# Performance work log

Measured on AMD Instinct MI355X. Metric: run time of the kernel, lower is better.

Reference implementation:

```python
import jax, jax.numpy as jnp
import numpy as np

B, S, D, H = 2, 2048, 1024, 16
HD = D // H  # 64


def setup_inputs() -> dict:
    key = jax.random.key(0)
    ks = jax.random.split(key, 10)
    inp = {
        "queries": jax.random.normal(ks[0], (B, S, D), dtype=jnp.float32),
        "keys": jax.random.normal(ks[1], (B, S, D), dtype=jnp.float32),
        "values": jax.random.normal(ks[2], (B, S, D), dtype=jnp.float32),
        "attention_mask": jax.random.randint(ks[3], (B, S), 0, 2, dtype=jnp.int32),
        # Linear params (torch nn.Linear: y = x @ W.T + b), scaled like default init
        "Wq": jax.random.normal(ks[4], (D, D), dtype=jnp.float32) / np.sqrt(D),
        "bq": jnp.zeros((D,), dtype=jnp.float32),
        "Wk": jax.random.normal(ks[5], (D, D), dtype=jnp.float32) / np.sqrt(D),
        "bk": jnp.zeros((D,), dtype=jnp.float32),
        "Wv": jax.random.normal(ks[6], (D, D), dtype=jnp.float32) / np.sqrt(D),
        "bv": jnp.zeros((D,), dtype=jnp.float32),
    }
    return inp


def _split_heads(x):
    # torch.chunk along last dim + stack(dim=1) == reshape + transpose
    b, s, d = x.shape
    return x.reshape(b, s, H, HD).transpose(0, 2, 1, 3)  # [B,H,S,hd]


def reference(queries, keys, values, attention_mask, Wq, bq, Wk, bk, Wv, bv):
    q = jax.nn.relu(queries @ Wq.T + bq)
    k = jax.nn.relu(keys @ Wk.T + bk)
    v = jax.nn.relu(values @ Wv.T + bv)
    qh, kh, vh = _split_heads(q), _split_heads(k), _split_heads(v)
    score = jnp.einsum("bhqd,bhkd->bhqk", qh, kh) / jnp.sqrt(jnp.float32(HD))
    # enc mask: [B,1,S,1] broadcast over key dim — masks whole query rows where mask==0
    row_mask = (attention_mask == 0)[:, None, :, None]
    score = jnp.where(row_mask, jnp.float32(-1e9), score)
    attn = jax.nn.softmax(score, axis=-1)
    a = jnp.einsum("bhqk,bhkd->bhqd", attn, vh)  # [B,H,S,hd]
    # faithful to original: permute(0,1,3,2) then reshape to (B,S,D)
    a = a.transpose(0, 1, 3, 2).reshape(q.shape[0], q.shape[1], q.shape[2])
    return a + queries
```

## Files before the change

### kernel.cpp

```cpp
#include <hip/hip_runtime.h>
#include <hip/hip_bf16.h>

#define DEV __device__ __forceinline__

typedef __attribute__((ext_vector_type(8))) short short8;
typedef __attribute__((ext_vector_type(4))) float f32x4;

#define MFMA16(a, b, c) __builtin_amdgcn_mfma_f32_16x16x32_bf16((a), (b), (c), 0, 0, 0)

static constexpr int B_ = 2, S_ = 2048, D_ = 1024, H_ = 16, HD_ = 64;
static constexpr long NX = (long)B_ * S_ * D_;
static constexpr long NW = (long)D_ * D_;

DEV short f2bf(float f) {
    __hip_bfloat16 h = __float2bfloat16(f);
    union { __hip_bfloat16 hh; short s; } u;
    u.hh = h;
    return u.s;
}

DEV float bf2f(short s) {
    union { float f; unsigned u; } x;
    x.u = ((unsigned)(unsigned short)s) << 16;
    return x.f;
}

DEV unsigned cvtpk(float a, float b) {
    unsigned r;
    asm("v_cvt_pk_bf16_f32 %0, %1, %2" : "=v"(r) : "v"(a), "v"(b));
    return r;
}

DEV short8 pk8(float4 lo, float4 hi) {
    union { short8 s8; unsigned u[4]; } u;
    u.u[0] = cvtpk(lo.x, lo.y);
    u.u[1] = cvtpk(lo.z, lo.w);
    u.u[2] = cvtpk(hi.x, hi.y);
    u.u[3] = cvtpk(hi.z, hi.w);
    return u.s8;
}

DEV short8 ld8(const short* p) { return *(const short8*)p; }

DEV void gld16(const short* g, short* l) {
    __builtin_amdgcn_global_load_lds(
        (const __attribute__((address_space(1))) unsigned int*)g,
        (__attribute__((address_space(3))) unsigned int*)l, 16, 0, 0);
}

__global__ __launch_bounds__(256) void convert_w(
    const float* __restrict__ wq, const float* __restrict__ wk, const float* __restrict__ wv,
    short* __restrict__ wqb, short* __restrict__ wkb, short* __restrict__ wvb) {
    long tid = (long)blockIdx.x * 256 + threadIdx.x;
    long e = tid * 4;
    const float* src; short* dst; long off;
    if      (e < NW)     { src = wq; dst = wqb; off = e; }
    else if (e < 2*NW)   { src = wk; dst = wkb; off = e - NW; }
    else                 { src = wv; dst = wvb; off = e - 2*NW; }
    float4 f = *(const float4*)(src + off);
    short4 o;
    o.x = f2bf(f.x); o.y = f2bf(f.y); o.z = f2bf(f.z); o.w = f2bf(f.w);
    *(short4*)(dst + off) = o;
}

__global__ __launch_bounds__(256) void gemm_bias_relu(
    const float* __restrict__ X0, const float* __restrict__ X1, const float* __restrict__ X2,
    const short* __restrict__ W0, const short* __restrict__ W1, const short* __restrict__ W2,
    const float* __restrict__ b0, const float* __restrict__ b1, const float* __restrict__ b2,
    short* __restrict__ O0, short* __restrict__ O1, short* __restrict__ O2) {
    __shared__ short As[2][128 * 32];
    __shared__ short Bs[2][128 * 32];

    const int bid = blockIdx.x;
    const int tl  = (bid & 7) * 96 + (bid >> 3);
    const int bx  = tl & 7;
    const int by  = (tl >> 3) & 31;
    const int z   = tl >> 8;

    const float* X   = (z == 0) ? X0 : (z == 1) ? X1 : X2;
    const short* W   = (z == 0) ? W0 : (z == 1) ? W1 : W2;
    const float* bia = (z == 0) ? b0 : (z == 1) ? b1 : b2;
    short*       Out = (z == 0) ? O0 : (z == 1) ? O1 : O2;

    const int tid  = threadIdx.x;
    const int wid  = tid >> 6;
    const int lane = tid & 63;
    const int id   = lane & 15;
    const int quad = lane >> 4;
    const int m0 = by * 128;
    const int n0 = bx * 128;
    const int wm = (wid >> 1) * 64;
    const int wn = (wid & 1) * 64;

    const float* Ag = X + (long)(m0 + wid * 32 + (lane >> 2)) * D_ + (lane & 3) * 8;
    const short* Bg0 = W + (long)(n0 + wid * 32 + (lane >> 2)) * D_ + (lane & 3) * 8;
    const int offW = wid * 1024;
    const int aDst = offW + lane * 8;

    f32x4 acc[4][4] = {};

    {
        float4 l0 = *(const float4*)(Ag);
        float4 h0 = *(const float4*)(Ag + 4);
        float4 l1 = *(const float4*)(Ag + 16 * D_);
        float4 h1 = *(const float4*)(Ag + 16 * D_ + 4);
        gld16(Bg0,            &Bs[0][offW]);
        gld16(Bg0 + 16 * D_,  &Bs[0][offW + 512]);
        *(short8*)(&As[0][aDst])       = pk8(l0, h0);
        *(short8*)(&As[0][aDst + 512]) = pk8(l1, h1);
    }

    for (int kk = 0; kk < D_; kk += 32) {
        const int cur = (kk >> 5) & 1;
        const int nxt = cur ^ 1;
        const bool pre = (kk + 32 < D_);
        float4 l0, h0, l1, h1;
        __syncthreads();
        if (pre) {
            l0 = *(const float4*)(Ag + kk + 32);
            h0 = *(const float4*)(Ag + kk + 36);
            l1 = *(const float4*)(Ag + 16 * D_ + kk + 32);
            h1 = *(const float4*)(Ag + 16 * D_ + kk + 36);
            gld16(Bg0 + kk + 32,            &Bs[nxt][offW]);
            gld16(Bg0 + 16 * D_ + kk + 32,  &Bs[nxt][offW + 512]);
        }

        short8 af[4], bf[4];
#pragma unroll
        for (int i = 0; i < 4; i++) af[i] = ld8(&As[cur][(wm + 16*i + id) * 32 + quad * 8]);
#pragma unroll
        for (int j = 0; j < 4; j++) bf[j] = ld8(&Bs[cur][(wn + 16*j + id) * 32 + quad * 8]);
#pragma unroll
        for (int i = 0; i < 4; i++)
#pragma unroll
            for (int j = 0; j < 4; j++)
                acc[i][j] = MFMA16(af[i], bf[j], acc[i][j]);

        if (pre) {
            *(short8*)(&As[nxt][aDst])       = pk8(l0, h0);
            *(short8*)(&As[nxt][aDst + 512]) = pk8(l1, h1);
        }
    }

#pragma unroll
    for (int j = 0; j < 4; j++) {
        int col = n0 + wn + 16*j + id;
        float bj = bia[col];
#pragma unroll
        for (int i = 0; i < 4; i++) {
#pragma unroll
            for (int r = 0; r < 4; r++) {
                int row = m0 + wm + 16*i + quad*4 + r;
                float val = fmaxf(acc[i][j][r] + bj, 0.f);
                Out[(long)row * D_ + col] = f2bf(val);
            }
        }
    }
}

__global__ __launch_bounds__(256) void transpose_v(const short* __restrict__ Vp,
                                                   short* __restrict__ VT) {
    __shared__ short tile[64 * 64];
    const int bh = blockIdx.y;
    const int b = bh >> 4, h = bh & 15;
    const int s0 = blockIdx.x * 64;
    const int t = threadIdx.x;
#pragma unroll
    for (int it = 0; it < 2; it++) {
        int row = (t >> 3) + 32 * it;
        int u   = t & 7;
        short8 d = ld8(Vp + (long)(b * S_ + s0 + row) * D_ + h * HD_ + u * 8);
        *(short8*)(&tile[row * 64 + (u ^ ((row >> 3) & 7)) * 8]) = d;
    }
    __syncthreads();
#pragma unroll
    for (int it = 0; it < 2; it++) {
        int e  = (t >> 3) + 32 * it;
        int sb = (t & 7) * 8;
        short8 o;
#pragma unroll
        for (int u = 0; u < 8; u++) {
            int row = sb + u;
            o[u] = tile[row * 64 + (((e >> 3) ^ ((row >> 3) & 7)) * 8) + (e & 7)];
        }
        *(short8*)(VT + ((long)bh * HD_ + e) * S_ + s0 + sb) = o;
    }
}

__global__ __launch_bounds__(256, 2) void attention(
    const short* __restrict__ Qb, const short* __restrict__ Kb,
    const short* __restrict__ VT, const int* __restrict__ mask,
    const float* __restrict__ queries, float* __restrict__ out) {
    __shared__ short Ks[2][64 * 64];
    __shared__ short Vs[2][64 * 64];
    __shared__ short pl[4][2 * 16 * 72];

    const int tid  = threadIdx.x;
    const int wid  = tid >> 6;
    const int lane = tid & 63;
    const int id   = lane & 15;
    const int quad = lane >> 4;

    const int bid = blockIdx.x;
    const int w   = bid >> 3;
    const int bh  = (bid & 7) + 8 * (w & 3);
    const int qt  = w >> 2;
    const int b   = bh >> 4;
    const int h   = bh & 15;
    const int q0  = qt * 128 + wid * 32;

    short8 qf[2][2];
#pragma unroll
    for (int g = 0; g < 2; g++) {
        const short* qbase = Qb + (long)(b * S_ + q0 + g * 16 + id) * D_ + h * HD_ + quad * 8;
        short8 f0 = ld8(qbase);
        short8 f1 = ld8(qbase + 32);
        const float qsc = mask[b * S_ + q0 + g * 16 + id] ? 0.125f : 0.f;
#pragma unroll
        for (int i = 0; i < 8; i++) {
            f0[i] = f2bf(bf2f(f0[i]) * qsc);
            f1[i] = f2bf(bf2f(f1[i]) * qsc);
        }
        qf[g][0] = f0; qf[g][1] = f1;
    }

    const int srow = wid * 16 + (lane >> 3);
    const int su   = (lane & 7) ^ (srow & 7);
    const short* kg0 = Kb + ((long)b * S_ + srow) * D_ + h * HD_ + su * 8;
    const short* vg0 = VT + (((long)(b * H_ + h) * HD_) + srow) * S_ + su * 8;
    short* plw = pl[wid];

    const int swz = id & 7;

    float l4[2][4] = {};
    f32x4 o[2][4] = {};

    gld16(kg0,            &Ks[0][wid * 1024]);
    gld16(kg0 + 8 * D_,   &Ks[0][wid * 1024 + 512]);
    gld16(vg0,            &Vs[0][wid * 1024]);
    gld16(vg0 + 8 * S_,   &Vs[0][wid * 1024 + 512]);

    for (int c0 = 0; c0 < S_; c0 += 64) {
        const int cur = (c0 >> 6) & 1;
        __syncthreads();
        if (c0 + 64 < S_) {
            const int nxt = cur ^ 1;
            const long cg = (long)(c0 + 64);
            gld16(kg0 + cg * D_,           &Ks[nxt][wid * 1024]);
            gld16(kg0 + cg * D_ + 8 * D_,  &Ks[nxt][wid * 1024 + 512]);
            gld16(vg0 + cg,                &Vs[nxt][wid * 1024]);
            gld16(vg0 + cg + 8 * S_,       &Vs[nxt][wid * 1024 + 512]);
        }

        f32x4 s[2][4];
#pragma unroll
        for (int g = 0; g < 2; g++)
#pragma unroll
            for (int t = 0; t < 4; t++) s[g][t] = (f32x4){0.f, 0.f, 0.f, 0.f};
#pragma unroll
        for (int t = 0; t < 4; t++) {
            short8 a0 = ld8(&Ks[cur][(16*t + id) * 64 + ((quad    ) ^ swz) * 8]);
            short8 a1 = ld8(&Ks[cur][(16*t + id) * 64 + ((quad ^ 4) ^ swz) * 8]);
            s[0][t] = MFMA16(a0, qf[0][0], s[0][t]);
            s[0][t] = MFMA16(a1, qf[0][1], s[0][t]);
            s[1][t] = MFMA16(a0, qf[1][0], s[1][t]);
            s[1][t] = MFMA16(a1, qf[1][1], s[1][t]);
        }

#pragma unroll
        for (int g = 0; g < 2; g++) {
            short* plg = plw + g * (16 * 72);
#pragma unroll
            for (int t = 0; t < 4; t++) {
                float p0 = __expf(s[g][t][0]);
                float p1 = __expf(s[g][t][1]);
                float p2 = __expf(s[g][t][2]);
                float p3 = __expf(s[g][t][3]);
                l4[g][0] += p0; l4[g][1] += p1; l4[g][2] += p2; l4[g][3] += p3;
                uint2 w2;
                w2.x = cvtpk(p0, p1);
                w2.y = cvtpk(p2, p3);
                *(uint2*)(&plg[id * 72 + 16 * t + quad * 4]) = w2;
            }
        }
        short8 pf[2][2];
#pragma unroll
        for (int g = 0; g < 2; g++) {
            short* plg = plw + g * (16 * 72);
            pf[g][0] = ld8(&plg[id * 72 + quad * 8]);
            pf[g][1] = ld8(&plg[id * 72 + 32 + quad * 8]);
        }

#pragma unroll
        for (int j2 = 0; j2 < 4; j2++) {
#pragma unroll
            for (int kh = 0; kh < 2; kh++) {
                short8 va = ld8(&Vs[cur][(16*j2 + id) * 64 + (((kh << 2) + quad) ^ swz) * 8]);
                o[0][j2] = MFMA16(va, pf[0][kh], o[0][j2]);
                o[1][j2] = MFMA16(va, pf[1][kh], o[1][j2]);
            }
        }
    }

    const long obase = (long)b * (S_ * D_) + (long)h * (HD_ * S_);
#pragma unroll
    for (int g = 0; g < 2; g++) {
        float l = l4[g][0] + l4[g][1] + l4[g][2] + l4[g][3];
        l += __shfl_xor(l, 16);
        l += __shfl_xor(l, 32);
        const float linv = 1.f / l;
#pragma unroll
        for (int j2 = 0; j2 < 4; j2++) {
#pragma unroll
            for (int r = 0; r < 4; r++) {
                int dim = 16 * j2 + quad * 4 + r;
                long idx = obase + (long)dim * S_ + q0 + g * 16 + id;
                out[idx] = o[g][j2][r] * linv + queries[idx];
            }
        }
    }
}

extern "C" void kernel_launch(void* const* d_in, const int* in_sizes, int n_in,
                              void* d_out, int out_size, void* d_ws, size_t ws_size,
                              hipStream_t stream) {
    const float* queries = (const float*)d_in[0];
    const float* keys    = (const float*)d_in[1];
    const float* values  = (const float*)d_in[2];
    const int*   mask    = (const int*)d_in[3];
    const float* Wq = (const float*)d_in[4];
    const float* bq = (const float*)d_in[5];
    const float* Wk = (const float*)d_in[6];
    const float* bk = (const float*)d_in[7];
    const float* Wv = (const float*)d_in[8];
    const float* bv = (const float*)d_in[9];
    float* out = (float*)d_out;

    short* ws  = (short*)d_ws;
    short* wqb = ws;
    short* wkb = wqb + NW;
    short* wvb = wkb + NW;
    short* Q   = wvb + NW;
    short* K   = Q   + NX;
    short* Vp  = K   + NX;
    short* VT  = Vp  + NX;

    convert_w<<<3072, 256, 0, stream>>>(Wq, Wk, Wv, wqb, wkb, wvb);
    gemm_bias_relu<<<768, 256, 0, stream>>>(queries, keys, values, wqb, wkb, wvb,
                                            bq, bk, bv, Q, K, Vp);
    transpose_v<<<dim3(32, 32), 256, 0, stream>>>(Vp, VT);
    attention<<<512, 256, 0, stream>>>(Q, K, VT, mask, queries, out);
}
```

Before: 238.8 us.

## Stream fp32 A tiles directly into LDS with swizzle, convert at fragment load

The projection GEMM now brings fp32 activation tiles into LDS with asynchronous global_load_lds, using an XOR swizzle on 4-float chunks. Each wave then converts to bf16 as it reads its MFMA fragments. This removes the register-staged global loads and the pack-and-store into LDS for A, so the prefetch overlaps compute without holding registers. In exchange, A's LDS footprint doubles, which may lower occupancy. The bf16 conversion is also repeated by each wave that shares the same A rows, on every k-step.

```diff
diff --git a/kernel.cpp b/kernel.cpp
--- a/kernel.cpp
+++ b/kernel.cpp
@@ -31,18 +31,19 @@
     return r;
 }
 
-DEV short8 pk8(float4 lo, float4 hi) {
+DEV short8 pk8(f32x4 lo, f32x4 hi) {
     union { short8 s8; unsigned u[4]; } u;
-    u.u[0] = cvtpk(lo.x, lo.y);
-    u.u[1] = cvtpk(lo.z, lo.w);
-    u.u[2] = cvtpk(hi.x, hi.y);
-    u.u[3] = cvtpk(hi.z, hi.w);
+    u.u[0] = cvtpk(lo[0], lo[1]);
+    u.u[1] = cvtpk(lo[2], lo[3]);
+    u.u[2] = cvtpk(hi[0], hi[1]);
+    u.u[3] = cvtpk(hi[2], hi[3]);
     return u.s8;
 }
 
 DEV short8 ld8(const short* p) { return *(const short8*)p; }
-
-DEV void gld16(const short* g, short* l) {
+DEV f32x4 ldf4(const float* p) { return *(const f32x4*)p; }
+
+DEV void gld16(const void* g, void* l) {
     __builtin_amdgcn_global_load_lds(
         (const __attribute__((address_space(1))) unsigned int*)g,
         (__attribute__((address_space(3))) unsigned int*)l, 16, 0, 0);
@@ -68,8 +69,8 @@
     const short* __restrict__ W0, const short* __restrict__ W1, const short* __restrict__ W2,
     const float* __restrict__ b0, const float* __restrict__ b1, const float* __restrict__ b2,
     short* __restrict__ O0, short* __restrict__ O1, short* __restrict__ O2) {
-    __shared__ short As[2][128 * 32];
-    __shared__ short Bs[2][128 * 32];
+    __shared__ __align__(16) float As[2][128 * 32];
+    __shared__ __align__(16) short Bs[2][128 * 32];
 
     const int bid = blockIdx.x;
     const int tl  = (bid & 7) * 96 + (bid >> 3);
@@ -92,42 +93,41 @@
     const int wm = (wid >> 1) * 64;
     const int wn = (wid & 1) * 64;
 
-    const float* Ag = X + (long)(m0 + wid * 32 + (lane >> 2)) * D_ + (lane & 3) * 8;
+    const int su = (lane & 7) ^ (lane >> 3);
+    const float* Agf = X + (long)(m0 + wid * 32 + (lane >> 3)) * D_ + su * 4;
     const short* Bg0 = W + (long)(n0 + wid * 32 + (lane >> 2)) * D_ + (lane & 3) * 8;
-    const int offW = wid * 1024;
-    const int aDst = offW + lane * 8;
+    const int offWA = wid * 1024;
+    const int offWB = wid * 1024;
+
+#define STAGE(buf, kk_)                                             \
+    do {                                                            \
+        gld16(Agf + (kk_),               &As[buf][offWA]);          \
+        gld16(Agf + (kk_) +  8 * D_,     &As[buf][offWA + 256]);    \
+        gld16(Agf + (kk_) + 16 * D_,     &As[buf][offWA + 512]);    \
+        gld16(Agf + (kk_) + 24 * D_,     &As[buf][offWA + 768]);    \
+        gld16(Bg0 + (kk_),               &Bs[buf][offWB]);          \
+        gld16(Bg0 + (kk_) + 16 * D_,     &Bs[buf][offWB + 512]);    \
+    } while (0)
 
     f32x4 acc[4][4] = {};
 
-    {
-        float4 l0 = *(const float4*)(Ag);
-        float4 h0 = *(const float4*)(Ag + 4);
-        float4 l1 = *(const float4*)(Ag + 16 * D_);
-        float4 h1 = *(const float4*)(Ag + 16 * D_ + 4);
-        gld16(Bg0,            &Bs[0][offW]);
-        gld16(Bg0 + 16 * D_,  &Bs[0][offW + 512]);
-        *(short8*)(&As[0][aDst])       = pk8(l0, h0);
-        *(short8*)(&As[0][aDst + 512]) = pk8(l1, h1);
-    }
+    STAGE(0, 0);
 
     for (int kk = 0; kk < D_; kk += 32) {
         const int cur = (kk >> 5) & 1;
-        const int nxt = cur ^ 1;
-        const bool pre = (kk + 32 < D_);
-        float4 l0, h0, l1, h1;
         __syncthreads();
-        if (pre) {
-            l0 = *(const float4*)(Ag + kk + 32);
-            h0 = *(const float4*)(Ag + kk + 36);
-            l1 = *(const float4*)(Ag + 16 * D_ + kk + 32);
-            h1 = *(const float4*)(Ag + 16 * D_ + kk + 36);
-            gld16(Bg0 + kk + 32,            &Bs[nxt][offW]);
-            gld16(Bg0 + 16 * D_ + kk + 32,  &Bs[nxt][offW + 512]);
-        }
+        if (kk + 32 < D_) STAGE(cur ^ 1, kk + 32);
 
         short8 af[4], bf[4];
 #pragma unroll
-        for (int i = 0; i < 4; i++) af[i] = ld8(&As[cur][(wm + 16*i + id) * 32 + quad * 8]);
+        for (int i = 0; i < 4; i++) {
+            const int r = wm + 16 * i + id;
+            const int u0 = (quad * 2) ^ (id & 7);
+            const float* rb = &As[cur][r * 32];
+            f32x4 lo = ldf4(rb + u0 * 4);
+            f32x4 hi = ldf4(rb + (u0 ^ 1) * 4);
+            af[i] = pk8(lo, hi);
+        }
 #pragma unroll
         for (int j = 0; j < 4; j++) bf[j] = ld8(&Bs[cur][(wn + 16*j + id) * 32 + quad * 8]);
 #pragma unroll
@@ -135,12 +135,8 @@
 #pragma unroll
             for (int j = 0; j < 4; j++)
                 acc[i][j] = MFMA16(af[i], bf[j], acc[i][j]);
-
-        if (pre) {
-            *(short8*)(&As[nxt][aDst])       = pk8(l0, h0);
-            *(short8*)(&As[nxt][aDst + 512]) = pk8(l1, h1);
-        }
-    }
+    }
+#undef STAGE
 
 #pragma unroll
     for (int j = 0; j < 4; j++) {
```

Result: faster. 198.3 us (-17.0%).
